# Kernel tuning notes

Measured on AMD Instinct MI355X. Metric: run time of the kernel, lower is better.

Reference implementation:

```python
import jax, jax.numpy as jnp
import numpy as np

DIM = 1024
NHEADS = 16
HEAD_DIM = DIM // NHEADS


def setup_inputs() -> dict:
    key = jax.random.key(0)
    ks = jax.random.split(key, 11)
    B, S = 4, 2048
    scale = 1.0 / np.sqrt(DIM)
    inp = {
        "Q": jax.random.normal(ks[0], (B, S, DIM), jnp.float32),
        "K": jax.random.normal(ks[1], (B, S, DIM), jnp.float32),
        "V": jax.random.normal(ks[2], (B, S, DIM), jnp.float32),
        "Wq": jax.random.normal(ks[3], (DIM, DIM), jnp.float32) * scale,
        "bq": jnp.zeros((DIM,), jnp.float32),
        "Wk": jax.random.normal(ks[4], (DIM, DIM), jnp.float32) * scale,
        "bk": jnp.zeros((DIM,), jnp.float32),
        "Wv": jax.random.normal(ks[5], (DIM, DIM), jnp.float32) * scale,
        "bv": jnp.zeros((DIM,), jnp.float32),
        "Wo": jax.random.normal(ks[6], (DIM, DIM), jnp.float32) * scale,
        "bo": jnp.zeros((DIM,), jnp.float32),
    }
    return inp


def _split_heads(x):
    # [B, S, D] -> [B, H, S, hd]
    B, S, _ = x.shape
    return x.reshape(B, S, NHEADS, HEAD_DIM).transpose(0, 2, 1, 3)


def reference(Q, K, V, Wq, bq, Wk, bk, Wv, bv, Wo, bo):
    q = _split_heads(Q @ Wq + bq)  # [B,H,S,hd]
    k = _split_heads(K @ Wk + bk)
    v = _split_heads(V @ Wv + bv)
    scores = jnp.einsum("bhqd,bhkd->bhqk", q, k) / np.sqrt(HEAD_DIM)
    attn = jax.nn.softmax(scores, axis=-1)  # dropout p=0 -> identity
    out = jnp.einsum("bhqk,bhkd->bhqd", attn, v)  # [B,H,S,hd]
    B, H, S, hd = out.shape
    out = out.transpose(0, 2, 1, 3).reshape(B, S, H * hd)
    return out @ Wo + bo
```

## Files before the change

### kernel.cpp

```cpp
#include <hip/hip_runtime.h>
#include <hip/hip_bf16.h>
#include <math.h>

#define DIM     1024
#define NHEADS  16
#define HD      64
#define BATCH   4
#define SEQ     2048
#define M_TOT   (BATCH * SEQ)
#define QSCALE  0.180336880111f

using short8 = __attribute__((ext_vector_type(8))) short;
using f32x4  = __attribute__((ext_vector_type(4))) float;

__device__ inline unsigned short f2bf(float x) {
    __hip_bfloat16 h = __float2bfloat16(x);
    unsigned short u;
    __builtin_memcpy(&u, &h, sizeof(u));
    return u;
}
__device__ inline void st_o(float* p, float v)          { *p = v; }
__device__ inline void st_o(unsigned short* p, float v) { *p = f2bf(v); }

__device__ inline void async16(const void* g, void* l) {
    __builtin_amdgcn_global_load_lds(
        (const __attribute__((address_space(1))) void*)g,
        (__attribute__((address_space(3))) void*)l, 16, 0, 0);
}

__global__ __launch_bounds__(256) void cvt3(
    const float* __restrict__ S0, const float* __restrict__ S1,
    const float* __restrict__ S2,
    unsigned short* __restrict__ D0, unsigned short* __restrict__ D1,
    unsigned short* __restrict__ D2)
{
    const float* src; unsigned short* dst;
    switch (blockIdx.y) {
        case 0:  src = S0; dst = D0; break;
        case 1:  src = S1; dst = D1; break;
        default: src = S2; dst = D2; break;
    }
    const size_t i = ((size_t)blockIdx.x * 256 + threadIdx.x) * 16;
    unsigned short tmp[16];
    #pragma unroll
    for (int p = 0; p < 4; ++p) {
        const float4 v = *(const float4*)(src + i + p * 4);
        tmp[p * 4 + 0] = f2bf(v.x); tmp[p * 4 + 1] = f2bf(v.y);
        tmp[p * 4 + 2] = f2bf(v.z); tmp[p * 4 + 3] = f2bf(v.w);
    }
    *(short8*)(dst + i)     = *(short8*)&tmp[0];
    *(short8*)(dst + i + 8) = *(short8*)&tmp[8];
}

__global__ __launch_bounds__(256) void wcvt4(
    const float* __restrict__ W0, const float* __restrict__ W1,
    const float* __restrict__ W2, const float* __restrict__ W3,
    unsigned short* __restrict__ T0, unsigned short* __restrict__ T1,
    unsigned short* __restrict__ T2, unsigned short* __restrict__ T3)
{
    const float* W; unsigned short* Wt;
    switch (blockIdx.z) {
        case 0:  W = W0; Wt = T0; break;
        case 1:  W = W1; Wt = T1; break;
        case 2:  W = W2; Wt = T2; break;
        default: W = W3; Wt = T3; break;
    }
    __shared__ unsigned short tile[32][33];
    const int t = threadIdx.x;
    const int tx = t & 31, ty = t >> 5;
    const int n0 = blockIdx.x * 32, k0 = blockIdx.y * 32;
    #pragma unroll
    for (int i = 0; i < 4; ++i) {
        const int kk = ty + i * 8;
        tile[kk][tx] = f2bf(W[(size_t)(k0 + kk) * DIM + n0 + tx]);
    }
    __syncthreads();
    #pragma unroll
    for (int i = 0; i < 4; ++i) {
        const int nn = ty + i * 8;
        Wt[(size_t)(n0 + nn) * DIM + k0 + tx] = tile[tx][nn];
    }
}

__global__ __launch_bounds__(256) void vtrans(const unsigned short* __restrict__ vf,
                                              unsigned short* __restrict__ vt) {
    __shared__ unsigned short tile[64][72];
    const int t = threadIdx.x;
    const int b = blockIdx.z, h = blockIdx.y, s0 = blockIdx.x * 64;
    const int r = t >> 2, c = (t & 3) * 16;
    const unsigned short* src = vf + (size_t)(b * SEQ + s0 + r) * DIM + h * HD + c;
    *(short8*)&tile[r][c]     = *(const short8*)src;
    *(short8*)&tile[r][c + 8] = *(const short8*)(src + 8);
    __syncthreads();
    unsigned short tmp[16];
    #pragma unroll
    for (int j = 0; j < 16; ++j) tmp[j] = tile[c + j][r];
    unsigned short* dst = vt + ((size_t)(b * NHEADS + h) * HD + r) * SEQ + s0 + c;
    *(short8*)dst       = *(short8*)&tmp[0];
    *(short8*)(dst + 8) = *(short8*)&tmp[8];
}

template <typename TY>
__global__ __launch_bounds__(256) void gemm_a16(
    const unsigned short* __restrict__ A, const unsigned short* __restrict__ Wt,
    const float* __restrict__ bias, TY* __restrict__ Y, float scale)
{
    __shared__ unsigned short As[128 * 32];
    __shared__ unsigned short Bs[128 * 32];
    const int t = threadIdx.x;
    const int lane = t & 63, wv = t >> 6;
    const int wm = wv >> 1, wn = wv & 1;
    const int l16 = lane & 15, lq = lane >> 4;
    const int m0 = blockIdx.y * 128, n0 = blockIdx.x * 128;
    const int lrow = lane >> 2;
    const int lcol = (lane & 3) * 8;

    f32x4 acc[4][4] = {};

    for (int k0 = 0; k0 < DIM; k0 += 32) {
        #pragma unroll
        for (int c = 0; c < 2; ++c) {
            const int ci  = wv * 2 + c;
            const int row = ci * 16 + lrow;
            async16(A  + (size_t)(m0 + row) * DIM + k0 + lcol, &As[ci * 512]);
            async16(Wt + (size_t)(n0 + row) * DIM + k0 + lcol, &Bs[ci * 512]);
        }
        __syncthreads();

        short8 af[4], bfr[4];
        #pragma unroll
        for (int mi = 0; mi < 4; ++mi)
            af[mi] = *(const short8*)&As[(wm * 64 + mi * 16 + l16) * 32 + lq * 8];
        #pragma unroll
        for (int nj = 0; nj < 4; ++nj)
            bfr[nj] = *(const short8*)&Bs[(wn * 64 + nj * 16 + l16) * 32 + lq * 8];
        #pragma unroll
        for (int mi = 0; mi < 4; ++mi)
            #pragma unroll
            for (int nj = 0; nj < 4; ++nj)
                acc[mi][nj] = __builtin_amdgcn_mfma_f32_16x16x32_bf16(
                    af[mi], bfr[nj], acc[mi][nj], 0, 0, 0);
        __syncthreads();
    }

    #pragma unroll
    for (int mi = 0; mi < 4; ++mi)
        #pragma unroll
        for (int nj = 0; nj < 4; ++nj) {
            const int row = m0 + wm * 64 + mi * 16 + lq * 4;
            const int col = n0 + wn * 64 + nj * 16 + l16;
            const float bb = bias[col];
            #pragma unroll
            for (int r = 0; r < 4; ++r)
                st_o(&Y[(size_t)(row + r) * DIM + col], (acc[mi][nj][r] + bb) * scale);
        }
}

__global__ __launch_bounds__(256) void attn_mfma(
    const unsigned short* qbuf, const unsigned short* __restrict__ kbuf,
    const unsigned short* __restrict__ vtb, unsigned short* ctx)
{
    __shared__ unsigned short Qs[64][72];
    __shared__ unsigned short Ks[64][72];
    __shared__ unsigned short Vs[64][72];
    __shared__ unsigned short Ps[64][72];

    const int t = threadIdx.x;
    const int lane = t & 63, wv = t >> 6;
    const int l16 = lane & 15, lq = lane >> 4;

    const unsigned lin  = (blockIdx.z * gridDim.y + blockIdx.y) * gridDim.x + blockIdx.x;
    const unsigned xcd  = lin & 7, slot = lin >> 3;
    const unsigned bh   = ((slot >> 5) << 3) | xcd;
    const int b = (int)(bh >> 4), h = (int)(bh & 15);
    const int q0 = (int)(slot & 31) * 64;

    const size_t base  = ((size_t)b * SEQ) * DIM + h * HD;
    const size_t vbase = ((size_t)(b * NHEADS + h)) * HD * SEQ;

    {
        const int r = t >> 2, c = (t & 3) * 16;
        const unsigned short* src = qbuf + base + (size_t)(q0 + r) * DIM + c;
        *(short8*)&Qs[r][c]     = *(const short8*)src;
        *(short8*)&Qs[r][c + 8] = *(const short8*)(src + 8);
    }
    const short8 aq0 = *(const short8*)&Qs[wv * 16 + l16][lq * 8];
    const short8 aq1 = *(const short8*)&Qs[wv * 16 + l16][32 + lq * 8];

    float l_part[4] = {0.f, 0.f, 0.f, 0.f};
    f32x4 O[4] = {};

    for (int s0 = 0; s0 < SEQ; s0 += 64) {
        __syncthreads();
        {
            const int r = t >> 2, c = (t & 3) * 16;
            const unsigned short* src = kbuf + base + (size_t)(s0 + r) * DIM + c;
            *(short8*)&Ks[r][c]     = *(const short8*)src;
            *(short8*)&Ks[r][c + 8] = *(const short8*)(src + 8);
        }
        {
            const int d = t >> 2, c = (t & 3) * 16;
            const unsigned short* src = vtb + vbase + (size_t)d * SEQ + s0 + c;
            *(short8*)&Vs[d][c]     = *(const short8*)src;
            *(short8*)&Vs[d][c + 8] = *(const short8*)(src + 8);
        }
        __syncthreads();

        f32x4 sa[4] = {};
        #pragma unroll
        for (int ti = 0; ti < 4; ++ti) {
            const short8 bk0 = *(const short8*)&Ks[ti * 16 + l16][lq * 8];
            const short8 bk1 = *(const short8*)&Ks[ti * 16 + l16][32 + lq * 8];
            sa[ti] = __builtin_amdgcn_mfma_f32_16x16x32_bf16(aq0, bk0, sa[ti], 0, 0, 0);
            sa[ti] = __builtin_amdgcn_mfma_f32_16x16x32_bf16(aq1, bk1, sa[ti], 0, 0, 0);
        }

        #pragma unroll
        for (int r = 0; r < 4; ++r) {
            const float v0 = __builtin_amdgcn_exp2f(sa[0][r]);
            const float v1 = __builtin_amdgcn_exp2f(sa[1][r]);
            const float v2 = __builtin_amdgcn_exp2f(sa[2][r]);
            const float v3 = __builtin_amdgcn_exp2f(sa[3][r]);
            l_part[r] += (v0 + v1) + (v2 + v3);
            const int prow = wv * 16 + lq * 4 + r;
            Ps[prow][l16]      = f2bf(v0);
            Ps[prow][16 + l16] = f2bf(v1);
            Ps[prow][32 + l16] = f2bf(v2);
            Ps[prow][48 + l16] = f2bf(v3);
        }

        #pragma unroll
        for (int kp = 0; kp < 2; ++kp) {
            const short8 ap = *(const short8*)&Ps[wv * 16 + l16][kp * 32 + lq * 8];
            #pragma unroll
            for (int dt = 0; dt < 4; ++dt) {
                const short8 bv = *(const short8*)&Vs[dt * 16 + l16][kp * 32 + lq * 8];
                O[dt] = __builtin_amdgcn_mfma_f32_16x16x32_bf16(ap, bv, O[dt], 0, 0, 0);
            }
        }
    }

    #pragma unroll
    for (int r = 0; r < 4; ++r) {
        float l = l_part[r];
        #pragma unroll
        for (int msk = 1; msk < 16; msk <<= 1) l += __shfl_xor(l, msk);
        const float inv = 1.0f / l;
        const int orow = wv * 16 + lq * 4 + r;
        #pragma unroll
        for (int dt = 0; dt < 4; ++dt)
            Ps[orow][dt * 16 + l16] = f2bf(O[dt][r] * inv);
    }
    __syncthreads();
    {
        const int r = t >> 2, c = (t & 3) * 16;
        unsigned short* dst = ctx + base + (size_t)(q0 + r) * DIM + c;
        *(short8*)dst       = *(const short8*)&Ps[r][c];
        *(short8*)(dst + 8) = *(const short8*)&Ps[r][c + 8];
    }
}

extern "C" void kernel_launch(void* const* d_in, const int* in_sizes, int n_in,
                              void* d_out, int out_size, void* d_ws, size_t ws_size,
                              hipStream_t stream) {
    const float* Q  = (const float*)d_in[0];
    const float* K  = (const float*)d_in[1];
    const float* V  = (const float*)d_in[2];
    const float* Wq = (const float*)d_in[3];
    const float* bq = (const float*)d_in[4];
    const float* Wk = (const float*)d_in[5];
    const float* bk = (const float*)d_in[6];
    const float* Wv = (const float*)d_in[7];
    const float* bv = (const float*)d_in[8];
    const float* Wo = (const float*)d_in[9];
    const float* bo = (const float*)d_in[10];
    float* out = (float*)d_out;

    const size_t eW = (size_t)DIM * DIM;
    const size_t eB = (size_t)M_TOT * DIM;
    unsigned short* p   = (unsigned short*)d_ws;
    unsigned short* wtq = p; p += eW;
    unsigned short* wtk = p; p += eW;
    unsigned short* wtv = p; p += eW;
    unsigned short* wto = p; p += eW;
    unsigned short* bufA = p; p += eB;
    unsigned short* bufB = p; p += eB;
    unsigned short* bufC = p; p += eB;
    unsigned short* bufD = p; p += eB;
    unsigned short* bufE = p;

    wcvt4<<<dim3(32, 32, 4), 256, 0, stream>>>(Wq, Wk, Wv, Wo, wtq, wtk, wtv, wto);

    const int cvt_blocks = (int)(eB / (256 * 16));
    cvt3<<<dim3(cvt_blocks, 3), 256, 0, stream>>>(V, Q, K, bufA, bufC, bufB);

    const dim3 gg(DIM / 128, M_TOT / 128);

    gemm_a16<unsigned short><<<gg, 256, 0, stream>>>(bufA, wtv, bv, bufD, 1.0f);
    vtrans<<<dim3(SEQ / 64, NHEADS, BATCH), 256, 0, stream>>>(bufD, bufE);
    gemm_a16<unsigned short><<<gg, 256, 0, stream>>>(bufC, wtq, bq, bufA, QSCALE);
    gemm_a16<unsigned short><<<gg, 256, 0, stream>>>(bufB, wtk, bk, bufD, 1.0f);

    attn_mfma<<<dim3(SEQ / 64, NHEADS, BATCH), 256, 0, stream>>>(bufA, bufD, bufE, bufA);

    gemm_a16<float><<<gg, 256, 0, stream>>>(bufA, wto, bo, out, 1.0f);
}
```

Baseline: 419.1 us.

## Double-buffer K/V with async LDS loads, keep P in registers, merge Q/K GEMMs

The attention kernel now loads K and V tiles with async global-to-LDS copies into double buffers using an XOR swizzle, which replaces the padded synchronous loads and drops one barrier per iteration. It computes S transposed (K as the A operand) so the exponentiated probabilities stay in registers and feed a 16x16x16 bf16 MFMA directly, removing the Ps LDS round trip. The row sums are reduced with fewer shuffles. The Q and K projection GEMMs are merged into a single launch with grid z=2, which cuts launch overhead and improves occupancy, at the cost of more per-block branching on the selected pointers.

```diff
diff --git a/kernel.cpp b/kernel.cpp
--- a/kernel.cpp
+++ b/kernel.cpp
@@ -11,6 +11,7 @@
 #define QSCALE  0.180336880111f
 
 using short8 = __attribute__((ext_vector_type(8))) short;
+using bf16x4 = __attribute__((ext_vector_type(4))) short;
 using f32x4  = __attribute__((ext_vector_type(4))) float;
 
 __device__ inline unsigned short f2bf(float x) {
@@ -101,12 +102,11 @@
 }
 
 template <typename TY>
-__global__ __launch_bounds__(256) void gemm_a16(
-    const unsigned short* __restrict__ A, const unsigned short* __restrict__ Wt,
-    const float* __restrict__ bias, TY* __restrict__ Y, float scale)
-{
-    __shared__ unsigned short As[128 * 32];
-    __shared__ unsigned short Bs[128 * 32];
+__device__ __forceinline__ void gemm_body(
+    const unsigned short* A, const unsigned short* Wt,
+    const float* bias, TY* Y, float scale,
+    unsigned short* As, unsigned short* Bs)
+{
     const int t = threadIdx.x;
     const int lane = t & 63, wv = t >> 6;
     const int wm = wv >> 1, wn = wv & 1;
@@ -156,18 +156,42 @@
         }
 }
 
+template <typename TY>
+__global__ __launch_bounds__(256) void gemm_a16(
+    const unsigned short* __restrict__ A, const unsigned short* __restrict__ Wt,
+    const float* __restrict__ bias, TY* __restrict__ Y, float scale)
+{
+    __shared__ unsigned short As[128 * 32];
+    __shared__ unsigned short Bs[128 * 32];
+    gemm_body<TY>(A, Wt, bias, Y, scale, As, Bs);
+}
+
+__global__ __launch_bounds__(256) void gemm_qk(
+    const unsigned short* Aq, const unsigned short* Wtq, const float* bq_,
+    unsigned short* Yq,
+    const unsigned short* Ak, const unsigned short* Wtk, const float* bk_,
+    unsigned short* Yk)
+{
+    __shared__ unsigned short As[128 * 32];
+    __shared__ unsigned short Bs[128 * 32];
+    const bool k = blockIdx.z != 0;
+    gemm_body<unsigned short>(k ? Ak : Aq, k ? Wtk : Wtq, k ? bk_ : bq_,
+                              k ? Yk : Yq, k ? 1.0f : QSCALE, As, Bs);
+}
+
 __global__ __launch_bounds__(256) void attn_mfma(
     const unsigned short* qbuf, const unsigned short* __restrict__ kbuf,
     const unsigned short* __restrict__ vtb, unsigned short* ctx)
 {
+    __shared__ unsigned short Kls[2 * 64 * 64];
+    __shared__ unsigned short Vls[2 * 64 * 64];
     __shared__ unsigned short Qs[64][72];
-    __shared__ unsigned short Ks[64][72];
-    __shared__ unsigned short Vs[64][72];
-    __shared__ unsigned short Ps[64][72];
 
     const int t = threadIdx.x;
     const int lane = t & 63, wv = t >> 6;
     const int l16 = lane & 15, lq = lane >> 4;
+    const int l7 = l16 & 7;
+    const int lqh = lq >> 1, lql4 = (lq & 1) * 4;
 
     const unsigned lin  = (blockIdx.z * gridDim.y + blockIdx.y) * gridDim.x + blockIdx.x;
     const unsigned xcd  = lin & 7, slot = lin >> 3;
@@ -178,85 +202,98 @@
     const size_t base  = ((size_t)b * SEQ) * DIM + h * HD;
     const size_t vbase = ((size_t)(b * NHEADS + h)) * HD * SEQ;
 
+    const int rl   = lane >> 3;
+    const int gcol = ((lane & 7) ^ rl) << 3;
+
     {
         const int r = t >> 2, c = (t & 3) * 16;
         const unsigned short* src = qbuf + base + (size_t)(q0 + r) * DIM + c;
         *(short8*)&Qs[r][c]     = *(const short8*)src;
         *(short8*)&Qs[r][c + 8] = *(const short8*)(src + 8);
     }
-    const short8 aq0 = *(const short8*)&Qs[wv * 16 + l16][lq * 8];
-    const short8 aq1 = *(const short8*)&Qs[wv * 16 + l16][32 + lq * 8];
-
-    float l_part[4] = {0.f, 0.f, 0.f, 0.f};
+    const short8 qf0 = *(const short8*)&Qs[wv * 16 + l16][lq * 8];
+    const short8 qf1 = *(const short8*)&Qs[wv * 16 + l16][32 + lq * 8];
+
+    float l_acc = 0.f;
     f32x4 O[4] = {};
 
+    #pragma unroll
+    for (int c = 0; c < 2; ++c) {
+        const int ci = wv * 2 + c;
+        async16(kbuf + base + (size_t)(ci * 8 + rl) * DIM + gcol, Kls + ci * 512);
+        async16(vtb + vbase + (size_t)(ci * 8 + rl) * SEQ + gcol, Vls + ci * 512);
+    }
+    __syncthreads();
+
+    int cur = 0;
     for (int s0 = 0; s0 < SEQ; s0 += 64) {
-        __syncthreads();
-        {
-            const int r = t >> 2, c = (t & 3) * 16;
-            const unsigned short* src = kbuf + base + (size_t)(s0 + r) * DIM + c;
-            *(short8*)&Ks[r][c]     = *(const short8*)src;
-            *(short8*)&Ks[r][c + 8] = *(const short8*)(src + 8);
-        }
-        {
-            const int d = t >> 2, c = (t & 3) * 16;
-            const unsigned short* src = vtb + vbase + (size_t)d * SEQ + s0 + c;
-            *(short8*)&Vs[d][c]     = *(const short8*)src;
-            *(short8*)&Vs[d][c + 8] = *(const short8*)(src + 8);
-        }
-        __syncthreads();
+        const unsigned short* Kc = Kls + cur * 4096;
+        const unsigned short* Vc = Vls + cur * 4096;
+
+        if (s0 + 64 < SEQ) {
+            unsigned short* Kd = Kls + (cur ^ 1) * 4096;
+            unsigned short* Vd = Vls + (cur ^ 1) * 4096;
+            #pragma unroll
+            for (int c = 0; c < 2; ++c) {
+                const int ci = wv * 2 + c;
+                async16(kbuf + base + (size_t)(s0 + 64 + ci * 8 + rl) * DIM + gcol,
+                        Kd + ci * 512);
+                async16(vtb + vbase + (size_t)(ci * 8 + rl) * SEQ + s0 + 64 + gcol,
+                        Vd + ci * 512);
+            }
+        }
 
         f32x4 sa[4] = {};
         #pragma unroll
         for (int ti = 0; ti < 4; ++ti) {
-            const short8 bk0 = *(const short8*)&Ks[ti * 16 + l16][lq * 8];
-            const short8 bk1 = *(const short8*)&Ks[ti * 16 + l16][32 + lq * 8];
-            sa[ti] = __builtin_amdgcn_mfma_f32_16x16x32_bf16(aq0, bk0, sa[ti], 0, 0, 0);
-            sa[ti] = __builtin_amdgcn_mfma_f32_16x16x32_bf16(aq1, bk1, sa[ti], 0, 0, 0);
-        }
-
-        #pragma unroll
-        for (int r = 0; r < 4; ++r) {
-            const float v0 = __builtin_amdgcn_exp2f(sa[0][r]);
-            const float v1 = __builtin_amdgcn_exp2f(sa[1][r]);
-            const float v2 = __builtin_amdgcn_exp2f(sa[2][r]);
-            const float v3 = __builtin_amdgcn_exp2f(sa[3][r]);
-            l_part[r] += (v0 + v1) + (v2 + v3);
-            const int prow = wv * 16 + lq * 4 + r;
-            Ps[prow][l16]      = f2bf(v0);
-            Ps[prow][16 + l16] = f2bf(v1);
-            Ps[prow][32 + l16] = f2bf(v2);
-            Ps[prow][48 + l16] = f2bf(v3);
-        }
-
-        #pragma unroll
-        for (int kp = 0; kp < 2; ++kp) {
-            const short8 ap = *(const short8*)&Ps[wv * 16 + l16][kp * 32 + lq * 8];
+            const int rr = ti * 16 + l16;
+            const short8 kf0 = *(const short8*)(Kc + rr * 64 + ((lq ^ l7) << 3));
+            const short8 kf1 = *(const short8*)(Kc + rr * 64 + (((4 + lq) ^ l7) << 3));
+            sa[ti] = __builtin_amdgcn_mfma_f32_16x16x32_bf16(kf0, qf0, sa[ti], 0, 0, 0);
+            sa[ti] = __builtin_amdgcn_mfma_f32_16x16x32_bf16(kf1, qf1, sa[ti], 0, 0, 0);
+        }
+
+        #pragma unroll
+        for (int ti = 0; ti < 4; ++ti) {
+            const float v0 = __builtin_amdgcn_exp2f(sa[ti][0]);
+            const float v1 = __builtin_amdgcn_exp2f(sa[ti][1]);
+            const float v2 = __builtin_amdgcn_exp2f(sa[ti][2]);
+            const float v3 = __builtin_amdgcn_exp2f(sa[ti][3]);
+            l_acc += (v0 + v1) + (v2 + v3);
+            bf16x4 pa;
+            pa[0] = (short)f2bf(v0); pa[1] = (short)f2bf(v1);
+            pa[2] = (short)f2bf(v2); pa[3] = (short)f2bf(v3);
             #pragma unroll
             for (int dt = 0; dt < 4; ++dt) {
-                const short8 bv = *(const short8*)&Vs[dt * 16 + l16][kp * 32 + lq * 8];
-                O[dt] = __builtin_amdgcn_mfma_f32_16x16x32_bf16(ap, bv, O[dt], 0, 0, 0);
+                const int vr = dt * 16 + l16;
+                const bf16x4 vb = *(const bf16x4*)(
+                    Vc + vr * 64 + (((2 * ti + lqh) ^ l7) << 3) + lql4);
+                O[dt] = __builtin_amdgcn_mfma_f32_16x16x16bf16_1k(pa, vb, O[dt], 0, 0, 0);
             }
         }
-    }
-
+
+        __syncthreads();
+        cur ^= 1;
+    }
+
+    l_acc += __shfl_xor(l_acc, 16);
+    l_acc += __shfl_xor(l_acc, 32);
+
+    unsigned short (*Ol)[72] = (unsigned short(*)[72])Kls;
     #pragma unroll
     for (int r = 0; r < 4; ++r) {
-        float l = l_part[r];
-        #pragma unroll
-        for (int msk = 1; msk < 16; msk <<= 1) l += __shfl_xor(l, msk);
-        const float inv = 1.0f / l;
+        const float inv = 1.0f / __shfl(l_acc, lq * 4 + r);
         const int orow = wv * 16 + lq * 4 + r;
         #pragma unroll
         for (int dt = 0; dt < 4; ++dt)
-            Ps[orow][dt * 16 + l16] = f2bf(O[dt][r] * inv);
+            Ol[orow][dt * 16 + l16] = f2bf(O[dt][r] * inv);
     }
     __syncthreads();
     {
         const int r = t >> 2, c = (t & 3) * 16;
         unsigned short* dst = ctx + base + (size_t)(q0 + r) * DIM + c;
-        *(short8*)dst       = *(const short8*)&Ps[r][c];
-        *(short8*)(dst + 8) = *(const short8*)&Ps[r][c + 8];
+        *(short8*)dst       = *(const short8*)&Ol[r][c];
+        *(short8*)(dst + 8) = *(const short8*)&Ol[r][c + 8];
     }
 }
 
@@ -298,8 +335,9 @@
 
     gemm_a16<unsigned short><<<gg, 256, 0, stream>>>(bufA, wtv, bv, bufD, 1.0f);
     vtrans<<<dim3(SEQ / 64, NHEADS, BATCH), 256, 0, stream>>>(bufD, bufE);
-    gemm_a16<unsigned short><<<gg, 256, 0, stream>>>(bufC, wtq, bq, bufA, QSCALE);
-    gemm_a16<unsigned short><<<gg, 256, 0, stream>>>(bufB, wtk, bk, bufD, 1.0f);
+    gemm_qk<<<dim3(DIM / 128, M_TOT / 128, 2), 256, 0, stream>>>(
+        bufC, wtq, bq, bufA,
+        bufB, wtk, bk, bufD);
 
     attn_mfma<<<dim3(SEQ / 64, NHEADS, BATCH), 256, 0, stream>>>(bufA, bufD, bufE, bufA);
 
```

After: 408.5 us. 1.03x faster.
